# Kernel optimization log

Measured on AMD Instinct MI355X. Metric: run time of the kernel, lower is better.

The kernel has to match this reference:

```python
import jax, jax.numpy as jnp
import numpy as np

B, S, H = 2, 1024, 2048
NH, NKV, HD = 16, 4, 128           # heads, kv heads, head_dim
E, TOPK, NG, TOPKG, M = 8, 2, 4, 2, 512  # experts, top_k, n_group, topk_group, moe ffn dim
EPS = 1e-6
THETA = 10000.0
SCALE = HD ** -0.5
RSF = 1.0  # routed_scaling_factor


def rmsnorm(x, w):
    xf = x.astype(jnp.float32)
    var = jnp.mean(xf * xf, axis=-1, keepdims=True)
    return (w * (xf * jax.lax.rsqrt(var + EPS))).astype(x.dtype)


def rotate_half(x):
    x1, x2 = jnp.split(x, 2, axis=-1)
    return jnp.concatenate([-x2, x1], axis=-1)


def setup_inputs() -> dict:
    key = jax.random.key(0)
    ks = jax.random.split(key, 16)
    s = 0.02
    hidden_states = jax.random.normal(ks[0], (B, S, H), jnp.float32)
    pos = jnp.arange(S, dtype=jnp.float32)
    inv_freq = 1.0 / (THETA ** (jnp.arange(0, HD, 2, dtype=jnp.float32) / HD))
    freqs = jnp.outer(pos, inv_freq)                       # [S, HD/2]
    emb = jnp.concatenate([freqs, freqs], axis=-1)         # [S, HD]
    cos = jnp.broadcast_to(jnp.cos(emb)[None], (B, S, HD))
    sin = jnp.broadcast_to(jnp.sin(emb)[None], (B, S, HD))
    return {
        "hidden_states": hidden_states,
        "cos": cos,
        "sin": sin,
        "ln1_w": jnp.ones((H,), jnp.float32),
        "w_qkv": jax.random.normal(ks[1], ((NH + 2 * NKV) * HD, H), jnp.float32) * s,
        "q_ln_w": jnp.ones((HD,), jnp.float32),
        "k_ln_w": jnp.ones((HD,), jnp.float32),
        "w_dense": jax.random.normal(ks[2], (H, NH * HD), jnp.float32) * s,
        "ln2_w": jnp.ones((H,), jnp.float32),
        "gate_w": jax.random.normal(ks[3], (E, H), jnp.float32) * s,
        "gate_bias": jnp.zeros((E,), jnp.float32),
        "we_gate": jax.random.normal(ks[4], (E, M, H), jnp.float32) * s,
        "we_up": jax.random.normal(ks[5], (E, M, H), jnp.float32) * s,
        "we_down": jax.random.normal(ks[6], (E, H, M), jnp.float32) * s,
        "ws_gate": jax.random.normal(ks[7], (M, H), jnp.float32) * s,
        "ws_up": jax.random.normal(ks[8], (M, H), jnp.float32) * s,
        "ws_down": jax.random.normal(ks[9], (H, M), jnp.float32) * s,
    }


def reference(hidden_states, cos, sin, ln1_w, w_qkv, q_ln_w, k_ln_w, w_dense,
              ln2_w, gate_w, gate_bias, we_gate, we_up, we_down,
              ws_gate, ws_up, ws_down):
    # ---- attention block ----
    residual = hidden_states
    x = rmsnorm(hidden_states, ln1_w)
    qkv = jnp.einsum('bsh,oh->bso', x, w_qkv).reshape(B, S, NH + 2 * NKV, HD)
    q, k, v = jnp.split(qkv, [NH, NH + NKV], axis=2)
    q = q.transpose(0, 2, 1, 3)   # [B, NH,  S, HD]
    k = k.transpose(0, 2, 1, 3)   # [B, NKV, S, HD]
    v = v.transpose(0, 2, 1, 3)
    q = rmsnorm(q, q_ln_w)
    k = rmsnorm(k, k_ln_w)
    c, sn = cos[:, None], sin[:, None]  # [B,1,S,HD]
    q = q * c + rotate_half(q) * sn
    k = k * c + rotate_half(k) * sn
    n_rep = NH // NKV
    k = jnp.repeat(k, n_rep, axis=1)
    v = jnp.repeat(v, n_rep, axis=1)
    scores = jnp.einsum('bhqd,bhkd->bhqk', q, k) * SCALE
    attn = jax.nn.softmax(scores.astype(jnp.float32), axis=-1).astype(q.dtype)
    out = jnp.einsum('bhqk,bhkd->bhqd', attn, v)
    out = out.transpose(0, 2, 1, 3).reshape(B, S, NH * HD)
    attn_out = jnp.einsum('bso,ho->bsh', out, w_dense)
    hidden = residual + attn_out

    # ---- MoE block ----
    residual = hidden
    x = rmsnorm(hidden, ln2_w).reshape(B * S, H)
    T = B * S
    logits = jnp.einsum('th,eh->te', x.astype(jnp.float32), gate_w.astype(jnp.float32))
    scores = jax.nn.sigmoid(logits)
    scores_b = scores + gate_bias
    # group-limited routing: pick topk_group groups by sum of top-2 scores per group
    gsz = E // NG
    grp = scores_b.reshape(T, NG, gsz)
    top2 = jax.lax.top_k(grp, min(2, gsz))[0].sum(-1)      # [T, NG]
    _, gidx = jax.lax.top_k(top2, TOPKG)                   # [T, TOPKG]
    gmask = jnp.zeros((T, NG), scores.dtype).at[jnp.arange(T)[:, None], gidx].set(1.0)
    emask = jnp.repeat(gmask, gsz, axis=-1)                # [T, E]
    masked = jnp.where(emask > 0, scores_b, -jnp.inf)
    _, tidx = jax.lax.top_k(masked, TOPK)                  # [T, TOPK]
    tw = jnp.take_along_axis(scores, tidx, axis=-1)
    tw = tw / (tw.sum(-1, keepdims=True) + 1e-20) * RSF
    route = jnp.zeros((T, E), x.dtype).at[jnp.arange(T)[:, None], tidx].set(tw.astype(x.dtype))
    # dense all-expert compute, combined by (sparse) routing weights
    g = jnp.einsum('th,emh->tem', x, we_gate)
    u = jnp.einsum('th,emh->tem', x, we_up)
    he = jax.nn.silu(g) * u
    oe = jnp.einsum('tem,ehm->teh', he, we_down)
    moe = jnp.einsum('te,teh->th', route, oe)
    # shared expert
    sh = jnp.einsum('th,oh->to', jax.nn.silu(x @ ws_gate.T) * (x @ ws_up.T), ws_down)
    out = residual + (moe + sh).reshape(B, S, H)
    return out
```

## Files before the change

### kernel.cpp

```cpp
#include <hip/hip_runtime.h>
#include <cstdint>
#include <cstddef>

#define T_TOK 2048
#define H_DIM 2048
#define S_LEN 1024
#define HD 128
#define NH 16
#define NKV 4
#define QKV_O 3072
#define MM 512
#define EPS 1e-6f
#define ATT_SCALE 0.08838834764831845f

typedef __bf16 bf16x8 __attribute__((ext_vector_type(8)));
typedef __bf16 bf16x4 __attribute__((ext_vector_type(4)));
typedef float  f32x4  __attribute__((ext_vector_type(4)));

__device__ __forceinline__ __bf16 f2bf(float f) {
  unsigned u = __builtin_bit_cast(unsigned, f);
  u += 0x7fffu + ((u >> 16) & 1u);
  unsigned short h = (unsigned short)(u >> 16);
  return __builtin_bit_cast(__bf16, h);
}
__device__ __forceinline__ f32x4 fzero4() {
  f32x4 z; z[0] = 0.f; z[1] = 0.f; z[2] = 0.f; z[3] = 0.f; return z;
}
__device__ __forceinline__ void gld16(const __bf16* g, __bf16* l) {
  __builtin_amdgcn_global_load_lds(
      (const __attribute__((address_space(1))) unsigned int*)g,
      (__attribute__((address_space(3))) unsigned int*)l, 16, 0, 0);
}

__global__ __launch_bounds__(256) void wconv_k(
    const float* __restrict__ s0, const float* __restrict__ s1,
    const float* __restrict__ s2, const float* __restrict__ s3,
    const float* __restrict__ s4, const float* __restrict__ s5,
    const float* __restrict__ s6, const float* __restrict__ s7,
    __bf16* __restrict__ dst) {
  size_t e = ((size_t)blockIdx.x * 256 + threadIdx.x) * 4;
  const size_t E0 = 6291456, E1 = 10485760, E2 = 18874368, E3 = 27262976,
               E4 = 35651584, E5 = 36700160, E6 = 37748736;
  const float* src; size_t base;
  if      (e < E0) { src = s0; base = 0;  }
  else if (e < E1) { src = s1; base = E0; }
  else if (e < E2) { src = s2; base = E1; }
  else if (e < E3) { src = s3; base = E2; }
  else if (e < E4) { src = s4; base = E3; }
  else if (e < E5) { src = s5; base = E4; }
  else if (e < E6) { src = s6; base = E5; }
  else             { src = s7; base = E6; }
  float4 f = *(const float4*)(src + (e - base));
  bf16x4 o;
  o[0] = f2bf(f.x); o[1] = f2bf(f.y); o[2] = f2bf(f.z); o[3] = f2bf(f.w);
  *(bf16x4*)(dst + e) = o;
}

__global__ __launch_bounds__(256) void rmsnorm_k(const float* __restrict__ X,
                                                 const float* __restrict__ W,
                                                 __bf16* __restrict__ Y) {
  int t = blockIdx.x;
  int tid = threadIdx.x, lane = tid & 63, wid = tid >> 6;
  const float4* row = (const float4*)(X + (size_t)t * H_DIM);
  float4 v0 = row[tid], v1 = row[tid + 256];
  float ss = v0.x*v0.x + v0.y*v0.y + v0.z*v0.z + v0.w*v0.w
           + v1.x*v1.x + v1.y*v1.y + v1.z*v1.z + v1.w*v1.w;
  #pragma unroll
  for (int m = 1; m <= 32; m <<= 1) ss += __shfl_xor(ss, m, 64);
  __shared__ float red[4];
  if (lane == 0) red[wid] = ss;
  __syncthreads();
  float tot = red[0] + red[1] + red[2] + red[3];
  float sc = rsqrtf(tot * (1.f / H_DIM) + EPS);
  const float4* wp = (const float4*)W;
  float4 w0 = wp[tid], w1 = wp[tid + 256];
  bf16x4 o;
  o[0] = f2bf(v0.x*w0.x*sc); o[1] = f2bf(v0.y*w0.y*sc);
  o[2] = f2bf(v0.z*w0.z*sc); o[3] = f2bf(v0.w*w0.w*sc);
  *(bf16x4*)&Y[(size_t)t*H_DIM + tid*4] = o;
  o[0] = f2bf(v1.x*w1.x*sc); o[1] = f2bf(v1.y*w1.y*sc);
  o[2] = f2bf(v1.z*w1.z*sc); o[3] = f2bf(v1.w*w1.w*sc);
  *(bf16x4*)&Y[(size_t)t*H_DIM + 1024 + tid*4] = o;
}

template<int MODE>
__global__ __launch_bounds__(256) void gemm_nt(
    const __bf16* __restrict__ A, const __bf16* __restrict__ B,
    const __bf16* __restrict__ B2, float* __restrict__ C,
    __bf16* __restrict__ OB, const float* __restrict__ resid,
    const int* __restrict__ list, const signed char* __restrict__ jsl,
    const int* __restrict__ cnt, int N, int K) {
  int e  = (MODE == 2) ? (int)blockIdx.z : 0;
  int ne = (MODE == 2) ? ((e == 8) ? T_TOK : cnt[e]) : T_TOK;
  int m0 = blockIdx.y * 128;
  if (MODE == 2 && m0 >= ne) return;
  int n0 = blockIdx.x * 128;
  const __bf16* Ab = A;
  const __bf16* Bb = B;
  if (MODE == 2) {
    Ab = A + (size_t)e * T_TOK * MM;
    Bb = (e < 8) ? B + (size_t)e * H_DIM * MM : B2;
  }
  __shared__ __bf16 sA[128 * 64];
  __shared__ __bf16 sB[128 * 64];
  int tid = threadIdx.x, lane = tid & 63, wid = tid >> 6;
  int quad = lane >> 4, l16 = lane & 15;
  int wm = wid & 1, wn = wid >> 1;

  const __bf16* gA[4]; const __bf16* gB[4];
  #pragma unroll
  for (int i = 0; i < 4; i++) {
    int p = tid + 256 * i;
    int row = p >> 3, sc = p & 7, gc = sc ^ (row & 7);
    gA[i] = Ab + (size_t)(m0 + row) * K + gc * 8;
    gB[i] = Bb + (size_t)(n0 + row) * K + gc * 8;
  }
  f32x4 acc[4][4];
  #pragma unroll
  for (int i = 0; i < 4; i++)
    #pragma unroll
    for (int j = 0; j < 4; j++) acc[i][j] = fzero4();

  for (int k0 = 0; k0 < K; k0 += 64) {
    __syncthreads();
    #pragma unroll
    for (int i = 0; i < 4; i++) {
      gld16(gA[i] + k0, &sA[(tid + 256 * i) * 8]);
      gld16(gB[i] + k0, &sB[(tid + 256 * i) * 8]);
    }
    __syncthreads();
    #pragma unroll
    for (int ks = 0; ks < 64; ks += 32) {
      int cb = ks >> 3;
      bf16x8 aF[4], bF[4];
      #pragma unroll
      for (int mt = 0; mt < 4; mt++) {
        int row = wm * 64 + mt * 16 + l16;
        int pos = row * 8 + ((cb + quad) ^ (row & 7));
        aF[mt] = *(const bf16x8*)&sA[pos * 8];
      }
      #pragma unroll
      for (int nt = 0; nt < 4; nt++) {
        int row = wn * 64 + nt * 16 + l16;
        int pos = row * 8 + ((cb + quad) ^ (row & 7));
        bF[nt] = *(const bf16x8*)&sB[pos * 8];
      }
      #pragma unroll
      for (int mt = 0; mt < 4; mt++)
        #pragma unroll
        for (int nt = 0; nt < 4; nt++)
          acc[mt][nt] = __builtin_amdgcn_mfma_f32_16x16x32_bf16(
              aF[mt], bF[nt], acc[mt][nt], 0, 0, 0);
    }
  }
  #pragma unroll
  for (int mt = 0; mt < 4; mt++) {
    #pragma unroll
    for (int nt = 0; nt < 4; nt++) {
      #pragma unroll
      for (int r = 0; r < 4; r++) {
        int row_l = wm*64 + mt*16 + quad*4 + r;
        int col_l = wn*64 + nt*16 + l16;
        int grow = m0 + row_l, gcol = n0 + col_l;
        float val = acc[mt][nt][r];
        if (MODE == 0) {
          OB[(size_t)grow * N + gcol] = f2bf(val);
        } else if (MODE == 1) {
          C[(size_t)grow * H_DIM + gcol] = val + resid[(size_t)grow * H_DIM + gcol];
        } else {
          if (grow < ne) {
            int tk = list[e * T_TOK + grow];
            int j  = (e == 8) ? 2 : (int)jsl[e * T_TOK + grow];
            OB[((size_t)tk * 3 + j) * H_DIM + gcol] = f2bf(val);
          }
        }
      }
    }
  }
}

__global__ __launch_bounds__(256) void combine_k(const __bf16* __restrict__ buf,
                                                 float* __restrict__ out) {
  int t = blockIdx.x, tid = threadIdx.x;
  const __bf16* base = buf + (size_t)t * 3 * H_DIM;
  bf16x8 v0 = *(const bf16x8*)(base + tid * 8);
  bf16x8 v1 = *(const bf16x8*)(base + H_DIM + tid * 8);
  bf16x8 v2 = *(const bf16x8*)(base + 2 * H_DIM + tid * 8);
  float* o = out + (size_t)t * H_DIM + tid * 8;
  float4 a = *(float4*)o, b = *(float4*)(o + 4);
  a.x += (float)v0[0] + (float)v1[0] + (float)v2[0];
  a.y += (float)v0[1] + (float)v1[1] + (float)v2[1];
  a.z += (float)v0[2] + (float)v1[2] + (float)v2[2];
  a.w += (float)v0[3] + (float)v1[3] + (float)v2[3];
  b.x += (float)v0[4] + (float)v1[4] + (float)v2[4];
  b.y += (float)v0[5] + (float)v1[5] + (float)v2[5];
  b.z += (float)v0[6] + (float)v1[6] + (float)v2[6];
  b.w += (float)v0[7] + (float)v1[7] + (float)v2[7];
  *(float4*)o = a; *(float4*)(o + 4) = b;
}

__global__ __launch_bounds__(256) void rope_k(
    const __bf16* __restrict__ qkv, const float* __restrict__ qlw,
    const float* __restrict__ klw, const float* __restrict__ cosp,
    const float* __restrict__ sinp, __bf16* __restrict__ qb,
    __bf16* __restrict__ kb, __bf16* __restrict__ vb) {
  int bid = blockIdx.x;
  int t = bid / 6;
  int head = (bid % 6) * 4 + (threadIdx.x >> 6);
  int b = t >> 10, s = t & 1023;
  int d = threadIdx.x & 63;
  const __bf16* src = qkv + (size_t)t * QKV_O + head * HD;
  float x1 = (float)src[d], x2 = (float)src[d + 64];
  if (head < 20) {
    float ssq = x1*x1 + x2*x2;
    #pragma unroll
    for (int m = 1; m <= 32; m <<= 1) ssq += __shfl_xor(ssq, m, 64);
    float sc = rsqrtf(ssq * (1.f / HD) + EPS);
    const float* w = (head < 16) ? qlw : klw;
    x1 = x1 * sc * w[d];
    x2 = x2 * sc * w[d + 64];
    size_t cb = (size_t)t * HD;
    float c1 = cosp[cb + d], s1 = sinp[cb + d];
    float c2 = cosp[cb + d + 64], s2 = sinp[cb + d + 64];
    float o1 = x1 * c1 - x2 * s1;
    float o2 = x2 * c2 + x1 * s2;
    if (head < 16) {
      __bf16* dst = qb + (((size_t)(b * NH + head)) * S_LEN + s) * HD;
      dst[d] = f2bf(o1); dst[d + 64] = f2bf(o2);
    } else {
      int kv = head - 16;
      __bf16* dst = kb + (((size_t)(b * NKV + kv)) * S_LEN + s) * HD;
      dst[d] = f2bf(o1); dst[d + 64] = f2bf(o2);
    }
  } else {
    int kv = head - 20;
    __bf16* dst = vb + (((size_t)(b * NKV + kv)) * S_LEN + s) * HD;
    dst[d] = src[d]; dst[d + 64] = src[d + 64];
  }
}

__global__ __launch_bounds__(256) void vtrans_k(const __bf16* __restrict__ vb,
                                                __bf16* __restrict__ vt) {
  int s0 = blockIdx.x * 64, d0 = blockIdx.y * 64, g = blockIdx.z;
  __shared__ __bf16 sT[64 * 80];
  int tid = threadIdx.x;
  const __bf16* src = vb + (size_t)g * S_LEN * HD;
  #pragma unroll
  for (int i = 0; i < 2; i++) {
    int p = tid + 256 * i;
    int rs = p >> 3, cc = p & 7;
    bf16x8 v = *(const bf16x8*)(src + (size_t)(s0 + rs) * HD + d0 + cc * 8);
    #pragma unroll
    for (int j = 0; j < 8; j++) sT[(cc * 8 + j) * 80 + rs] = v[j];
  }
  __syncthreads();
  __bf16* dst = vt + (size_t)g * HD * S_LEN;
  #pragma unroll
  for (int i = 0; i < 2; i++) {
    int p = tid + 256 * i;
    int rd = p >> 3, cs = p & 7;
    bf16x8 v = *(const bf16x8*)&sT[rd * 80 + cs * 8];
    *(bf16x8*)(dst + (size_t)(d0 + rd) * S_LEN + s0 + cs * 8) = v;
  }
}

__global__ __launch_bounds__(256) void flash_k(
    const __bf16* __restrict__ qb, const __bf16* __restrict__ kb,
    const __bf16* __restrict__ vt, __bf16* __restrict__ outb) {
  int qt = blockIdx.x, bh = blockIdx.y;
  int b = bh >> 4, h = bh & 15, kv = h >> 2;
  int tid = threadIdx.x, lane = tid & 63, wid = tid >> 6;
  int quad = lane >> 4, l16 = lane & 15;
  __shared__ __bf16 sQ[64 * 128];
  __shared__ __bf16 sKP[64 * 128];
  __shared__ __bf16 sVt[128 * 64];
  __bf16* sK = sKP;
  __bf16* sP = sKP;

  const __bf16* qsrc = qb + (((size_t)(b * NH + h)) * S_LEN + qt * 64) * HD;
  #pragma unroll
  for (int i = 0; i < 4; i++) {
    int p = tid + 256 * i;
    int row = p >> 4, sc = p & 15, gc = sc ^ (row & 7);
    gld16(qsrc + (size_t)row * HD + gc * 8, &sQ[p * 8]);
  }
  const __bf16* kbase  = kb + ((size_t)(b * NKV + kv)) * S_LEN * HD;
  const __bf16* vtbase = vt + ((size_t)(b * NKV + kv)) * HD * S_LEN;
  const __bf16* gK[4]; const __bf16* gV[4];
  #pragma unroll
  for (int i = 0; i < 4; i++) {
    int p = tid + 256 * i;
    int rowk = p >> 4, sck = p & 15, gck = sck ^ (rowk & 7);
    gK[i] = kbase + (size_t)rowk * HD + gck * 8;
    int rowv = p >> 3, scv = p & 7, gcv = scv ^ (rowv & 7);
    gV[i] = vtbase + (size_t)rowv * S_LEN + gcv * 8;
  }
  float mrow[4], lrow[4];
  #pragma unroll
  for (int r = 0; r < 4; r++) { mrow[r] = -__builtin_inff(); lrow[r] = 0.f; }
  f32x4 accO[8];
  #pragma unroll
  for (int i = 0; i < 8; i++) accO[i] = fzero4();

  for (int kt = 0; kt < 16; kt++) {
    __syncthreads();
    #pragma unroll
    for (int i = 0; i < 4; i++) {
      gld16(gK[i] + (size_t)kt * 64 * HD, &sK[(tid + 256 * i) * 8]);
      gld16(gV[i] + kt * 64, &sVt[(tid + 256 * i) * 8]);
    }
    __syncthreads();
    f32x4 accS[4];
    #pragma unroll
    for (int jt = 0; jt < 4; jt++) accS[jt] = fzero4();
    int rowA = wid * 16 + l16;
    #pragma unroll
    for (int ks2 = 0; ks2 < 4; ks2++) {
      int posA = rowA * 16 + ((ks2 * 4 + quad) ^ (rowA & 7));
      bf16x8 aF = *(const bf16x8*)&sQ[posA * 8];
      #pragma unroll
      for (int jt = 0; jt < 4; jt++) {
        int rowB = jt * 16 + l16;
        int posB = rowB * 16 + ((ks2 * 4 + quad) ^ (rowB & 7));
        bf16x8 bF = *(const bf16x8*)&sK[posB * 8];
        accS[jt] = __builtin_amdgcn_mfma_f32_16x16x32_bf16(aF, bF, accS[jt], 0, 0, 0);
      }
    }
    float alpha[4];
    #pragma unroll
    for (int r = 0; r < 4; r++) {
      float mx = -__builtin_inff();
      #pragma unroll
      for (int jt = 0; jt < 4; jt++) {
        accS[jt][r] *= ATT_SCALE;
        mx = fmaxf(mx, accS[jt][r]);
      }
      #pragma unroll
      for (int m = 1; m <= 8; m <<= 1) mx = fmaxf(mx, __shfl_xor(mx, m, 64));
      float mn = fmaxf(mrow[r], mx);
      float al = __expf(mrow[r] - mn);
      float rs = 0.f;
      #pragma unroll
      for (int jt = 0; jt < 4; jt++) {
        float p = __expf(accS[jt][r] - mn);
        accS[jt][r] = p;
        rs += p;
      }
      #pragma unroll
      for (int m = 1; m <= 8; m <<= 1) rs += __shfl_xor(rs, m, 64);
      lrow[r] = lrow[r] * al + rs;
      mrow[r] = mn;
      alpha[r] = al;
    }
    #pragma unroll
    for (int nt = 0; nt < 8; nt++)
      #pragma unroll
      for (int r = 0; r < 4; r++) accO[nt][r] *= alpha[r];
    __syncthreads();
    #pragma unroll
    for (int jt = 0; jt < 4; jt++)
      #pragma unroll
      for (int r = 0; r < 4; r++)
        sP[(wid * 16 + quad * 4 + r) * 72 + jt * 16 + l16] = f2bf(accS[jt][r]);
    __syncthreads();
    #pragma unroll
    for (int ks2 = 0; ks2 < 2; ks2++) {
      bf16x8 aF = *(const bf16x8*)&sP[(wid * 16 + l16) * 72 + ks2 * 32 + quad * 8];
      #pragma unroll
      for (int nt = 0; nt < 8; nt++) {
        int rowB = nt * 16 + l16;
        int posB = rowB * 8 + ((ks2 * 4 + quad) ^ (rowB & 7));
        bf16x8 bF = *(const bf16x8*)&sVt[posB * 8];
        accO[nt] = __builtin_amdgcn_mfma_f32_16x16x32_bf16(aF, bF, accO[nt], 0, 0, 0);
      }
    }
  }
  #pragma unroll
  for (int nt = 0; nt < 8; nt++) {
    #pragma unroll
    for (int r = 0; r < 4; r++) {
      int srow = qt * 64 + wid * 16 + quad * 4 + r;
      float val = accO[nt][r] / lrow[r];
      outb[((size_t)(b * S_LEN + srow)) * H_DIM + h * HD + nt * 16 + l16] = f2bf(val);
    }
  }
}

__global__ __launch_bounds__(64) void router_k(
    const float* __restrict__ hid, const float* __restrict__ ln2w,
    const float* __restrict__ gw, const float* __restrict__ gb,
    int* __restrict__ cnt, int* __restrict__ list, float* __restrict__ wsl,
    signed char* __restrict__ jsl) {
  int t = blockIdx.x;
  int lane = threadIdx.x;
  const float* xr = hid + (size_t)t * H_DIM;
  float x[32];
  float ss = 0.f;
  #pragma unroll
  for (int j = 0; j < 32; j++) { x[j] = xr[j * 64 + lane]; ss += x[j] * x[j]; }
  #pragma unroll
  for (int m = 1; m <= 32; m <<= 1) ss += __shfl_xor(ss, m, 64);
  float sc = rsqrtf(ss * (1.f / H_DIM) + EPS);
  float xn[32];
  #pragma unroll
  for (int j = 0; j < 32; j++) xn[j] = x[j] * sc * ln2w[j * 64 + lane];
  float lg[8];
  #pragma unroll
  for (int e = 0; e < 8; e++) {
    float d = 0.f;
    #pragma unroll
    for (int j = 0; j < 32; j++) d += xn[j] * gw[(size_t)e * H_DIM + j * 64 + lane];
    #pragma unroll
    for (int m = 1; m <= 32; m <<= 1) d += __shfl_xor(d, m, 64);
    lg[e] = d;
  }
  float s[8], sb[8];
  #pragma unroll
  for (int e = 0; e < 8; e++) {
    s[e] = 1.f / (1.f + __expf(-lg[e]));
    sb[e] = s[e] + gb[e];
  }
  float gs[4];
  #pragma unroll
  for (int g = 0; g < 4; g++) gs[g] = sb[2 * g] + sb[2 * g + 1];
  int g1 = 0;
  for (int g = 1; g < 4; g++) if (gs[g] > gs[g1]) g1 = g;
  int g2 = -1;
  for (int g = 0; g < 4; g++) if (g != g1 && (g2 < 0 || gs[g] > gs[g2])) g2 = g;
  unsigned emask = (3u << (2 * g1)) | (3u << (2 * g2));
  int e1 = -1;
  for (int e = 0; e < 8; e++) if (((emask >> e) & 1u) && (e1 < 0 || sb[e] > sb[e1])) e1 = e;
  int e2 = -1;
  for (int e = 0; e < 8; e++) if (((emask >> e) & 1u) && e != e1 && (e2 < 0 || sb[e] > sb[e2])) e2 = e;
  float w1 = s[e1], w2 = s[e2];
  float dn = w1 + w2 + 1e-20f;
  w1 /= dn; w2 /= dn;
  if (lane == 0) {
    int p1 = atomicAdd(&cnt[e1], 1);
    list[e1 * T_TOK + p1] = t; wsl[e1 * T_TOK + p1] = w1; jsl[e1 * T_TOK + p1] = 0;
    int p2 = atomicAdd(&cnt[e2], 1);
    list[e2 * T_TOK + p2] = t; wsl[e2 * T_TOK + p2] = w2; jsl[e2 * T_TOK + p2] = 1;
    list[8 * T_TOK + t] = t; wsl[8 * T_TOK + t] = 1.f;
  }
}

__global__ __launch_bounds__(256) void gemm_gateup(
    const __bf16* __restrict__ X, const __bf16* __restrict__ weg,
    const __bf16* __restrict__ weu, const __bf16* __restrict__ wsg,
    const __bf16* __restrict__ wsu, const int* __restrict__ list,
    const float* __restrict__ wsl, const int* __restrict__ cnt,
    __bf16* __restrict__ he) {
  int e = blockIdx.z;
  int ne = (e == 8) ? T_TOK : cnt[e];
  int m0 = blockIdx.y * 128;
  if (m0 >= ne) return;
  int n0 = blockIdx.x * 64;
  const __bf16* bg = (e < 8) ? weg + (size_t)e * MM * H_DIM : wsg;
  const __bf16* bu = (e < 8) ? weu + (size_t)e * MM * H_DIM : wsu;
  const int* lst = list + e * T_TOK;
  __shared__ __bf16 sA[128 * 64];
  __shared__ __bf16 sBg[64 * 64];
  __shared__ __bf16 sBu[64 * 64];
  int tid = threadIdx.x, lane = tid & 63, wid = tid >> 6;
  int quad = lane >> 4, l16 = lane & 15;

  const __bf16* gA[4]; const __bf16* gBg[2]; const __bf16* gBu[2];
  #pragma unroll
  for (int i = 0; i < 4; i++) {
    int p = tid + 256 * i;
    int row = p >> 3, sc = p & 7, gc = sc ^ (row & 7);
    int r = m0 + row; if (r >= ne) r = ne - 1;
    int tk = lst[r];
    gA[i] = X + (size_t)tk * H_DIM + gc * 8;
  }
  #pragma unroll
  for (int i = 0; i < 2; i++) {
    int p = tid + 256 * i;
    int row = p >> 3, sc = p & 7, gc = sc ^ (row & 7);
    gBg[i] = bg + (size_t)(n0 + row) * H_DIM + gc * 8;
    gBu[i] = bu + (size_t)(n0 + row) * H_DIM + gc * 8;
  }
  f32x4 ag[2][4], au[2][4];
  #pragma unroll
  for (int i = 0; i < 2; i++)
    #pragma unroll
    for (int j = 0; j < 4; j++) { ag[i][j] = fzero4(); au[i][j] = fzero4(); }

  for (int k0 = 0; k0 < H_DIM; k0 += 64) {
    __syncthreads();
    #pragma unroll
    for (int i = 0; i < 4; i++)
      gld16(gA[i] + k0, &sA[(tid + 256 * i) * 8]);
    #pragma unroll
    for (int i = 0; i < 2; i++) {
      gld16(gBg[i] + k0, &sBg[(tid + 256 * i) * 8]);
      gld16(gBu[i] + k0, &sBu[(tid + 256 * i) * 8]);
    }
    __syncthreads();
    #pragma unroll
    for (int ks = 0; ks < 64; ks += 32) {
      int cb = ks >> 3;
      bf16x8 aF[2], gF[4], uF[4];
      #pragma unroll
      for (int mt = 0; mt < 2; mt++) {
        int row = wid * 32 + mt * 16 + l16;
        int pos = row * 8 + ((cb + quad) ^ (row & 7));
        aF[mt] = *(const bf16x8*)&sA[pos * 8];
      }
      #pragma unroll
      for (int nt = 0; nt < 4; nt++) {
        int row = nt * 16 + l16;
        int pos = row * 8 + ((cb + quad) ^ (row & 7));
        gF[nt] = *(const bf16x8*)&sBg[pos * 8];
        uF[nt] = *(const bf16x8*)&sBu[pos * 8];
      }
      #pragma unroll
      for (int mt = 0; mt < 2; mt++)
        #pragma unroll
        for (int nt = 0; nt < 4; nt++) {
          ag[mt][nt] = __builtin_amdgcn_mfma_f32_16x16x32_bf16(aF[mt], gF[nt], ag[mt][nt], 0, 0, 0);
          au[mt][nt] = __builtin_amdgcn_mfma_f32_16x16x32_bf16(aF[mt], uF[nt], au[mt][nt], 0, 0, 0);
        }
    }
  }
  #pragma unroll
  for (int mt = 0; mt < 2; mt++) {
    #pragma unroll
    for (int nt = 0; nt < 4; nt++) {
      #pragma unroll
      for (int r = 0; r < 4; r++) {
        int row_l = wid * 32 + mt * 16 + quad * 4 + r;
        int grow = m0 + row_l;
        if (grow < ne) {
          float g = ag[mt][nt][r], u = au[mt][nt][r];
          float hv = g / (1.f + __expf(-g)) * u;
          hv *= wsl[e * T_TOK + grow];
          he[((size_t)e * T_TOK + grow) * MM + n0 + nt * 16 + l16] = f2bf(hv);
        }
      }
    }
  }
}

extern "C" void kernel_launch(void* const* d_in, const int* in_sizes, int n_in,
                              void* d_out, int out_size, void* d_ws, size_t ws_size,
                              hipStream_t stream) {
  (void)in_sizes; (void)n_in; (void)out_size; (void)ws_size;
  const float* hs     = (const float*)d_in[0];
  const float* cosp   = (const float*)d_in[1];
  const float* sinp   = (const float*)d_in[2];
  const float* ln1w   = (const float*)d_in[3];
  const float* wqkv   = (const float*)d_in[4];
  const float* qlw    = (const float*)d_in[5];
  const float* klw    = (const float*)d_in[6];
  const float* wdense = (const float*)d_in[7];
  const float* ln2w   = (const float*)d_in[8];
  const float* gw     = (const float*)d_in[9];
  const float* gbias  = (const float*)d_in[10];
  const float* weg    = (const float*)d_in[11];
  const float* weu    = (const float*)d_in[12];
  const float* wed    = (const float*)d_in[13];
  const float* wsg    = (const float*)d_in[14];
  const float* wsu    = (const float*)d_in[15];
  const float* wsd    = (const float*)d_in[16];
  float* out = (float*)d_out;

  char* ws = (char*)d_ws;
  size_t off = 0;
  auto alloc = [&](size_t b) { char* p = ws + off; off += (b + 255) & ~(size_t)255; return p; };
  __bf16* wbf   = (__bf16*)alloc((size_t)38797312 * 2);
  __bf16* xb1   = (__bf16*)alloc((size_t)T_TOK * H_DIM * 2);
  __bf16* qreg  = (__bf16*)alloc((size_t)T_TOK * 3 * H_DIM * 2);
  __bf16* qb    = (__bf16*)alloc((size_t)2 * NH  * S_LEN * HD * 2);
  __bf16* kb    = (__bf16*)alloc((size_t)2 * NKV * S_LEN * HD * 2);
  __bf16* vb    = (__bf16*)alloc((size_t)2 * NKV * S_LEN * HD * 2);
  __bf16* vt    = (__bf16*)alloc((size_t)2 * NKV * S_LEN * HD * 2);
  __bf16* outb  = (__bf16*)alloc((size_t)T_TOK * H_DIM * 2);
  __bf16* xb2   = (__bf16*)alloc((size_t)T_TOK * H_DIM * 2);
  int*    cnt   = (int*)   alloc(256);
  int*    list  = (int*)   alloc((size_t)9 * T_TOK * 4);
  float*  wsl   = (float*) alloc((size_t)9 * T_TOK * 4);
  signed char* jsl = (signed char*)alloc((size_t)9 * T_TOK);
  __bf16* qkvb  = qreg;
  __bf16* buf   = qreg;
  __bf16* he    = qb;

  const __bf16* wqkv_bf   = wbf;
  const __bf16* wdense_bf = wbf + 6291456;
  const __bf16* weg_bf    = wbf + 10485760;
  const __bf16* weu_bf    = wbf + 18874368;
  const __bf16* wed_bf    = wbf + 27262976;
  const __bf16* wsg_bf    = wbf + 35651584;
  const __bf16* wsu_bf    = wbf + 36700160;
  const __bf16* wsd_bf    = wbf + 37748736;

  hipMemsetAsync(cnt, 0, 256, stream);
  wconv_k<<<37888, 256, 0, stream>>>(wqkv, wdense, weg, weu, wed, wsg, wsu, wsd, wbf);
  rmsnorm_k<<<T_TOK, 256, 0, stream>>>(hs, ln1w, xb1);
  gemm_nt<0><<<dim3(QKV_O / 128, T_TOK / 128), 256, 0, stream>>>(
      xb1, wqkv_bf, nullptr, nullptr, qkvb, nullptr, nullptr, nullptr, nullptr, QKV_O, H_DIM);
  rope_k<<<T_TOK * 6, 256, 0, stream>>>(qkvb, qlw, klw, cosp, sinp, qb, kb, vb);
  vtrans_k<<<dim3(16, 2, 8), 256, 0, stream>>>(vb, vt);
  flash_k<<<dim3(S_LEN / 64, 2 * NH), 256, 0, stream>>>(qb, kb, vt, outb);
  gemm_nt<1><<<dim3(H_DIM / 128, T_TOK / 128), 256, 0, stream>>>(
      outb, wdense_bf, nullptr, out, nullptr, hs, nullptr, nullptr, nullptr, H_DIM, H_DIM);
  rmsnorm_k<<<T_TOK, 256, 0, stream>>>(out, ln2w, xb2);
  router_k<<<T_TOK, 64, 0, stream>>>(out, ln2w, gw, gbias, cnt, list, wsl, jsl);
  gemm_gateup<<<dim3(MM / 64, T_TOK / 128, 9), 256, 0, stream>>>(
      xb2, weg_bf, weu_bf, wsg_bf, wsu_bf, list, wsl, cnt, he);
  gemm_nt<2><<<dim3(H_DIM / 128, T_TOK / 128, 9), 256, 0, stream>>>(
      he, wed_bf, wsd_bf, nullptr, buf, nullptr, list, jsl, cnt, H_DIM, MM);
  combine_k<<<T_TOK, 256, 0, stream>>>(buf, out);
}
```

Before: 528.3 us.

## Double-buffer LDS tiles in GEMM kernels and widen weight-conversion stores

The dense/expert GEMM and the fused gate-up GEMM now keep two LDS buffers. Each iteration issues the async global→LDS loads for the next K tile before running the MFMAs on the current tile, so loads overlap with compute, and one barrier per iteration is removed. This doubles LDS use per block, which may reduce occupancy. Separately, the fp32→bf16 weight conversion kernel now handles 8 elements per thread with 16-byte stores and launches half as many blocks.

```diff
diff --git a/kernel.cpp b/kernel.cpp
--- a/kernel.cpp
+++ b/kernel.cpp
@@ -38,7 +38,7 @@
     const float* __restrict__ s4, const float* __restrict__ s5,
     const float* __restrict__ s6, const float* __restrict__ s7,
     __bf16* __restrict__ dst) {
-  size_t e = ((size_t)blockIdx.x * 256 + threadIdx.x) * 4;
+  size_t e = ((size_t)blockIdx.x * 256 + threadIdx.x) * 8;
   const size_t E0 = 6291456, E1 = 10485760, E2 = 18874368, E3 = 27262976,
                E4 = 35651584, E5 = 36700160, E6 = 37748736;
   const float* src; size_t base;
@@ -50,10 +50,12 @@
   else if (e < E5) { src = s5; base = E4; }
   else if (e < E6) { src = s6; base = E5; }
   else             { src = s7; base = E6; }
-  float4 f = *(const float4*)(src + (e - base));
-  bf16x4 o;
-  o[0] = f2bf(f.x); o[1] = f2bf(f.y); o[2] = f2bf(f.z); o[3] = f2bf(f.w);
-  *(bf16x4*)(dst + e) = o;
+  const float4* sp = (const float4*)(src + (e - base));
+  float4 f0 = sp[0], f1 = sp[1];
+  bf16x8 o;
+  o[0] = f2bf(f0.x); o[1] = f2bf(f0.y); o[2] = f2bf(f0.z); o[3] = f2bf(f0.w);
+  o[4] = f2bf(f1.x); o[5] = f2bf(f1.y); o[6] = f2bf(f1.z); o[7] = f2bf(f1.w);
+  *(bf16x8*)(dst + e) = o;
 }
 
 __global__ __launch_bounds__(256) void rmsnorm_k(const float* __restrict__ X,
@@ -101,8 +103,8 @@
     Ab = A + (size_t)e * T_TOK * MM;
     Bb = (e < 8) ? B + (size_t)e * H_DIM * MM : B2;
   }
-  __shared__ __bf16 sA[128 * 64];
-  __shared__ __bf16 sB[128 * 64];
+  __shared__ __bf16 sA[2][128 * 64];
+  __shared__ __bf16 sB[2][128 * 64];
   int tid = threadIdx.x, lane = tid & 63, wid = tid >> 6;
   int quad = lane >> 4, l16 = lane & 15;
   int wm = wid & 1, wn = wid >> 1;
@@ -121,14 +123,18 @@
     #pragma unroll
     for (int j = 0; j < 4; j++) acc[i][j] = fzero4();
 
+  auto stage = [&](int buf, int k0) {
+    #pragma unroll
+    for (int i = 0; i < 4; i++) {
+      gld16(gA[i] + k0, &sA[buf][(tid + 256 * i) * 8]);
+      gld16(gB[i] + k0, &sB[buf][(tid + 256 * i) * 8]);
+    }
+  };
+  stage(0, 0);
+  int cur = 0;
   for (int k0 = 0; k0 < K; k0 += 64) {
     __syncthreads();
-    #pragma unroll
-    for (int i = 0; i < 4; i++) {
-      gld16(gA[i] + k0, &sA[(tid + 256 * i) * 8]);
-      gld16(gB[i] + k0, &sB[(tid + 256 * i) * 8]);
-    }
-    __syncthreads();
+    if (k0 + 64 < K) stage(cur ^ 1, k0 + 64);
     #pragma unroll
     for (int ks = 0; ks < 64; ks += 32) {
       int cb = ks >> 3;
@@ -137,13 +143,13 @@
       for (int mt = 0; mt < 4; mt++) {
         int row = wm * 64 + mt * 16 + l16;
         int pos = row * 8 + ((cb + quad) ^ (row & 7));
-        aF[mt] = *(const bf16x8*)&sA[pos * 8];
+        aF[mt] = *(const bf16x8*)&sA[cur][pos * 8];
       }
       #pragma unroll
       for (int nt = 0; nt < 4; nt++) {
         int row = wn * 64 + nt * 16 + l16;
         int pos = row * 8 + ((cb + quad) ^ (row & 7));
-        bF[nt] = *(const bf16x8*)&sB[pos * 8];
+        bF[nt] = *(const bf16x8*)&sB[cur][pos * 8];
       }
       #pragma unroll
       for (int mt = 0; mt < 4; mt++)
@@ -152,6 +158,7 @@
           acc[mt][nt] = __builtin_amdgcn_mfma_f32_16x16x32_bf16(
               aF[mt], bF[nt], acc[mt][nt], 0, 0, 0);
     }
+    cur ^= 1;
   }
   #pragma unroll
   for (int mt = 0; mt < 4; mt++) {
@@ -458,9 +465,9 @@
   const __bf16* bg = (e < 8) ? weg + (size_t)e * MM * H_DIM : wsg;
   const __bf16* bu = (e < 8) ? weu + (size_t)e * MM * H_DIM : wsu;
   const int* lst = list + e * T_TOK;
-  __shared__ __bf16 sA[128 * 64];
-  __shared__ __bf16 sBg[64 * 64];
-  __shared__ __bf16 sBu[64 * 64];
+  __shared__ __bf16 sA[2][128 * 64];
+  __shared__ __bf16 sBg[2][64 * 64];
+  __shared__ __bf16 sBu[2][64 * 64];
   int tid = threadIdx.x, lane = tid & 63, wid = tid >> 6;
   int quad = lane >> 4, l16 = lane & 15;
 
@@ -486,17 +493,21 @@
     #pragma unroll
     for (int j = 0; j < 4; j++) { ag[i][j] = fzero4(); au[i][j] = fzero4(); }
 
+  auto stage = [&](int buf, int k0) {
+    #pragma unroll
+    for (int i = 0; i < 4; i++)
+      gld16(gA[i] + k0, &sA[buf][(tid + 256 * i) * 8]);
+    #pragma unroll
+    for (int i = 0; i < 2; i++) {
+      gld16(gBg[i] + k0, &sBg[buf][(tid + 256 * i) * 8]);
+      gld16(gBu[i] + k0, &sBu[buf][(tid + 256 * i) * 8]);
+    }
+  };
+  stage(0, 0);
+  int cur = 0;
   for (int k0 = 0; k0 < H_DIM; k0 += 64) {
     __syncthreads();
-    #pragma unroll
-    for (int i = 0; i < 4; i++)
-      gld16(gA[i] + k0, &sA[(tid + 256 * i) * 8]);
-    #pragma unroll
-    for (int i = 0; i < 2; i++) {
-      gld16(gBg[i] + k0, &sBg[(tid + 256 * i) * 8]);
-      gld16(gBu[i] + k0, &sBu[(tid + 256 * i) * 8]);
-    }
-    __syncthreads();
+    if (k0 + 64 < H_DIM) stage(cur ^ 1, k0 + 64);
     #pragma unroll
     for (int ks = 0; ks < 64; ks += 32) {
       int cb = ks >> 3;
@@ -505,14 +516,14 @@
       for (int mt = 0; mt < 2; mt++) {
         int row = wid * 32 + mt * 16 + l16;
         int pos = row * 8 + ((cb + quad) ^ (row & 7));
-        aF[mt] = *(const bf16x8*)&sA[pos * 8];
+        aF[mt] = *(const bf16x8*)&sA[cur][pos * 8];
       }
       #pragma unroll
       for (int nt = 0; nt < 4; nt++) {
         int row = nt * 16 + l16;
         int pos = row * 8 + ((cb + quad) ^ (row & 7));
-        gF[nt] = *(const bf16x8*)&sBg[pos * 8];
-        uF[nt] = *(const bf16x8*)&sBu[pos * 8];
+        gF[nt] = *(const bf16x8*)&sBg[cur][pos * 8];
+        uF[nt] = *(const bf16x8*)&sBu[cur][pos * 8];
       }
       #pragma unroll
       for (int mt = 0; mt < 2; mt++)
@@ -522,6 +533,7 @@
           au[mt][nt] = __builtin_amdgcn_mfma_f32_16x16x32_bf16(aF[mt], uF[nt], au[mt][nt], 0, 0, 0);
         }
     }
+    cur ^= 1;
   }
   #pragma unroll
   for (int mt = 0; mt < 2; mt++) {
@@ -595,7 +607,7 @@
   const __bf16* wsd_bf    = wbf + 37748736;
 
   hipMemsetAsync(cnt, 0, 256, stream);
-  wconv_k<<<37888, 256, 0, stream>>>(wqkv, wdense, weg, weu, wed, wsg, wsu, wsd, wbf);
+  wconv_k<<<18944, 256, 0, stream>>>(wqkv, wdense, weg, weu, wed, wsg, wsu, wsd, wbf);
   rmsnorm_k<<<T_TOK, 256, 0, stream>>>(hs, ln1w, xb1);
   gemm_nt<0><<<dim3(QKV_O / 128, T_TOK / 128), 256, 0, stream>>>(
       xb1, wqkv_bf, nullptr, nullptr, qkvb, nullptr, nullptr, nullptr, nullptr, QKV_O, H_DIM);
```

New measurement: 526.5 us. About the same (-0.3%).
